# Performance work log

Hardware: AMD Instinct MI355X
Metric: run time of the kernel (lower is better)

## Reference

```python
import jax, jax.numpy as jnp
import numpy as np

EMBED_DIM = 2048
HEAD_DIM = 128
B, T = 4, 2048


def setup_inputs() -> dict:
    key = jax.random.key(0)
    k1, k2, k3, k4 = jax.random.split(key, 4)
    x_in = jax.random.normal(k1, (B, T, EMBED_DIM), dtype=jnp.float32)
    scale = 1.0 / np.sqrt(EMBED_DIM)
    Wq = jax.random.normal(k2, (EMBED_DIM, HEAD_DIM), dtype=jnp.float32) * scale
    Wk = jax.random.normal(k3, (EMBED_DIM, HEAD_DIM), dtype=jnp.float32) * scale
    Wv = jax.random.normal(k4, (EMBED_DIM, HEAD_DIM), dtype=jnp.float32) * scale
    return {"x_in": x_in, "Wq": Wq, "Wk": Wk, "Wv": Wv}


def reference(x_in, Wq, Wk, Wv):
    # x_in: [B, T, E]; projections (Linear, no bias)
    q = jnp.einsum('bte,ed->btd', x_in, Wq)  # [B,T,D]
    k = jnp.einsum('bte,ed->btd', x_in, Wk)
    v = jnp.einsum('bte,ed->btd', x_in, Wv)
    t = x_in.shape[1]
    d = Wq.shape[1]
    s = jnp.einsum('btd,bsd->bts', q, k) / jnp.sqrt(jnp.asarray(d, q.dtype))  # [B,Tq,Tk]
    # causal mask: positions with tril==0 (k index > q index) -> -inf
    causal = jnp.tril(jnp.ones((t, t), dtype=bool))
    s = jnp.where(causal, s, -jnp.inf)
    # NOTE: original module applies softmax over dim=1 (query axis), faithfully reproduced
    a = jax.nn.softmax(s, axis=1)
    z = jnp.einsum('bts,bsd->btd', a, v)  # [B,T,D]
    return z
```

## Files before the change

### kernel.cpp

```cpp
#include <hip/hip_runtime.h>

typedef _Float16 f16x8 __attribute__((ext_vector_type(8)));
typedef _Float16 f16x4 __attribute__((ext_vector_type(4)));
typedef float f32x4 __attribute__((ext_vector_type(4)));

#define T_DIM 2048
#define E_DIM 2048
#define D_DIM 128
#define NB 4
#define KSP_P 4
#define KCH_P 512
#define KSP_A 8
#define KCH_A 256
#define NCH2 32

__device__ __forceinline__ void gll16(const void* g, void* l) {
  __builtin_amdgcn_global_load_lds(
      (const __attribute__((address_space(1))) unsigned int*)g,
      (__attribute__((address_space(3))) unsigned int*)l, 16, 0, 0);
}

__device__ __forceinline__ void merge_stat(float& m, float& l, float pm, float pl) {
  if (pm != -__builtin_inff()) {
    float nm = fmaxf(m, pm);
    l = l * __expf(m - nm) + pl * __expf(pm - nm);
    m = nm;
  }
}


__global__ void cvt_w(const float* __restrict__ Wq, const float* __restrict__ Wk,
                      const float* __restrict__ Wv, _Float16* __restrict__ WhT) {
  int idx = blockIdx.x * 256 + threadIdx.x;
  int w = blockIdx.y;
  const float* W = (w == 0) ? Wq : ((w == 1) ? Wk : Wv);
  int e = idx & (E_DIM - 1), d = idx >> 11;
  WhT[(size_t)w * (D_DIM * E_DIM) + idx] = (_Float16)W[e * D_DIM + d];
}


__global__ __launch_bounds__(768) void proj_gemm(
    const float* __restrict__ x, const _Float16* __restrict__ WhT,
    _Float16* __restrict__ Ph) {
  __shared__ _Float16 A16[2][128 * 32];
  __shared__ _Float16 Bsw[2][384 * 32];
  const int tid = threadIdx.x, w = tid >> 6, lane = tid & 63;
  const int wn = w >> 1, wr = w & 1, quad = lane >> 4, l16 = lane & 15;
  const int t0 = blockIdx.x * 128;
  const int ks = blockIdx.y;
  const int kb = ks * KCH_P;
  const int arowA = tid >> 2, asegA = tid & 3;
  const int br = tid >> 2, bseg = tid & 3;

  f32x4 ax0, ax1;
  auto loadA = [&](int k0) {
    if (tid < 512) {
      const float* src = x + (size_t)(t0 + arowA) * E_DIM + k0 + asegA * 8;
      ax0 = *(const f32x4*)src;
      ax1 = *(const f32x4*)(src + 4);
    }
  };
  auto writeA = [&](int buf) {
    if (tid < 512) {
      f16x8 o;
#pragma unroll
      for (int e = 0; e < 4; ++e) {
        o[e] = (_Float16)ax0[e];
        o[e + 4] = (_Float16)ax1[e];
      }
      *(f16x8*)(&A16[buf][arowA * 32 + asegA * 8]) = o;
    }
  };
  auto stageB = [&](int buf, int k0) {
    int g = bseg ^ ((br >> 1) & 3);
    gll16(WhT + (size_t)br * E_DIM + k0 + g * 8, &Bsw[buf][br * 32 + bseg * 8]);
    int r = 192 + br;
    int g2 = bseg ^ ((r >> 1) & 3);
    gll16(WhT + (size_t)r * E_DIM + k0 + g2 * 8, &Bsw[buf][r * 32 + bseg * 8]);
  };

  f32x4 acc[4][4] = {};
  loadA(kb);
  stageB(0, kb);
  asm volatile("s_waitcnt vmcnt(0)" ::: "memory");
  writeA(0);
  const int NIT = KCH_P / 32;
  for (int it = 0; it < NIT; ++it) {
    const int cur = it & 1;
    __syncthreads();
    if (it + 1 < NIT) {
      loadA(kb + (it + 1) * 32);
      stageB(cur ^ 1, kb + (it + 1) * 32);
    }
    f16x8 af[4], bf[4];
#pragma unroll
    for (int i = 0; i < 4; ++i) {
      int row = wr * 64 + i * 16 + l16;
      af[i] = *(const f16x8*)(&A16[cur][row * 32 + quad * 8]);
    }
#pragma unroll
    for (int j = 0; j < 4; ++j) {
      int row = wn * 64 + j * 16 + l16;
      int sg = quad ^ ((row >> 1) & 3);
      bf[j] = *(const f16x8*)(&Bsw[cur][row * 32 + sg * 8]);
    }
    __builtin_amdgcn_s_setprio(1);
#pragma unroll
    for (int i = 0; i < 4; ++i)
#pragma unroll
      for (int j = 0; j < 4; ++j)
        acc[i][j] = __builtin_amdgcn_mfma_f32_16x16x32_f16(af[i], bf[j], acc[i][j], 0, 0, 0);
    __builtin_amdgcn_s_setprio(0);
    if (it + 1 < NIT) {
      asm volatile("s_waitcnt vmcnt(0)" ::: "memory");
      writeA(cur ^ 1);
    }
  }
  const int mat = wn >> 1;
  const int nb0 = (wn & 1) * 64;
  _Float16* P = Ph + ((size_t)(ks * 3 + mat) << 20);
  if (mat < 2) {
#pragma unroll
    for (int i = 0; i < 4; ++i)
#pragma unroll
      for (int j = 0; j < 4; ++j) {
        int n = nb0 + j * 16 + l16;
#pragma unroll
        for (int r = 0; r < 4; ++r) {
          int t = t0 + wr * 64 + i * 16 + quad * 4 + r;
          P[(size_t)t * D_DIM + n] = (_Float16)acc[i][j][r];
        }
      }
  } else {
#pragma unroll
    for (int i = 0; i < 4; ++i)
#pragma unroll
      for (int j = 0; j < 4; ++j) {
        int n = nb0 + j * 16 + l16;
        int t = t0 + wr * 64 + i * 16 + quad * 4;
        f16x4 o;
#pragma unroll
        for (int r = 0; r < 4; ++r) o[r] = (_Float16)acc[i][j][r];
        *(f16x4*)(P + ((size_t)(t >> 11) * D_DIM + n) * T_DIM + (t & (T_DIM - 1))) = o;
      }
  }
}


__global__ void proj_reduce(const _Float16* __restrict__ Ph, _Float16* __restrict__ Qh,
                            _Float16* __restrict__ Kh, _Float16* __restrict__ VT) {
  size_t u = ((size_t)blockIdx.x * 256 + threadIdx.x) * 8;
  int mat = (int)(u >> 20);
  size_t rem = u & ((1u << 20) - 1);
  float s[8] = {};
#pragma unroll
  for (int ks = 0; ks < KSP_P; ++ks) {
    f16x8 p = *(const f16x8*)(Ph + ((size_t)(ks * 3 + mat) << 20) + rem);
#pragma unroll
    for (int e = 0; e < 8; ++e) s[e] += (float)p[e];
  }
  f16x8 o;
#pragma unroll
  for (int e = 0; e < 8; ++e) o[e] = (_Float16)s[e];
  _Float16* dst = (mat == 0) ? Qh : ((mat == 1) ? Kh : VT);
  *(f16x8*)(dst + rem) = o;
}


__global__ __launch_bounds__(256) void s_gemm(const _Float16* __restrict__ Qh,
                                              const _Float16* __restrict__ Kh,
                                              _Float16* __restrict__ S,
                                              float* __restrict__ Pm,
                                              float* __restrict__ Pl) {
  int idx = blockIdx.x;
  int xt = (int)((sqrtf(8.f * idx + 1.f) - 1.f) * 0.5f);
  while ((xt + 1) * (xt + 2) / 2 <= idx) ++xt;
  while (xt * (xt + 1) / 2 > idx) --xt;
  int yt = idx - xt * (xt + 1) / 2;
  __shared__ _Float16 Bs[4][128 * 32];
  const int tid = threadIdx.x, w = tid >> 6, lane = tid & 63;
  const int wr = w >> 1, wc = w & 1, quad = lane >> 4, l16 = lane & 15;
  const int t0 = xt * 128, s0 = yt * 128, b = blockIdx.y;
  const _Float16* A = Qh + (size_t)b * T_DIM * D_DIM;
  const _Float16* B = Kh + (size_t)b * T_DIM * D_DIM;
  const int srow = lane >> 2;
  const int swz = ((lane & 3) ^ ((srow >> 1) & 3)) * 8;
#pragma unroll
  for (int kq = 0; kq < 4; ++kq)
#pragma unroll
    for (int q = 0; q < 2; ++q) {
      int rbase = w * 32 + q * 16;
      gll16(B + (size_t)(s0 + rbase + srow) * D_DIM + kq * 32 + swz,
            Bs[kq] + rbase * 32);
    }
  __syncthreads();
  f32x4 acc[4][4] = {};
  const int bsg = (quad ^ ((l16 >> 1) & 3)) * 8;
#pragma unroll
  for (int kq = 0; kq < 4; ++kq) {
    f16x8 af[4], bf[4];
#pragma unroll
    for (int i = 0; i < 4; ++i)
      af[i] = *(const f16x8*)(A + (size_t)(t0 + wr * 64 + i * 16 + l16) * D_DIM +
                              kq * 32 + quad * 8);
#pragma unroll
    for (int j = 0; j < 4; ++j)
      bf[j] = *(const f16x8*)(Bs[kq] + (wc * 64 + j * 16 + l16) * 32 + bsg);
#pragma unroll
    for (int i = 0; i < 4; ++i)
#pragma unroll
      for (int j = 0; j < 4; ++j)
        acc[i][j] = __builtin_amdgcn_mfma_f32_16x16x32_f16(af[i], bf[j], acc[i][j], 0, 0, 0);
  }
  _Float16* Sb = S + (size_t)b * T_DIM * T_DIM;
  const float scale = 0.08838834764831845f;
  const float NEG = -__builtin_inff();
#pragma unroll
  for (int j = 0; j < 4; ++j) {
    const int s = s0 + wc * 64 + j * 16 + l16;
    float vv[16];
    float m = NEG;
#pragma unroll
    for (int i = 0; i < 4; ++i)
#pragma unroll
      for (int r = 0; r < 4; ++r) {
        int t = t0 + wr * 64 + i * 16 + quad * 4 + r;
        float v = (s > t) ? NEG : acc[i][j][r] * scale;
        Sb[(size_t)t * T_DIM + s] = (_Float16)v;
        vv[i * 4 + r] = v;
        m = fmaxf(m, v);
      }
    float l = 0.f;
    if (m != NEG) {
#pragma unroll
      for (int k = 0; k < 16; ++k) l += __expf(vv[k] - m);
    }
#pragma unroll
    for (int d = 16; d <= 32; d <<= 1) {
      float pm = __shfl_xor(m, d, 64);
      float pl = __shfl_xor(l, d, 64);
      merge_stat(m, l, pm, pl);
    }
    if (quad == 0) {
      int c = 2 * xt + wr;
      Pm[((size_t)c * NB + b) * T_DIM + s] = m;
      Pl[((size_t)c * NB + b) * T_DIM + s] = l;
    }
  }
}


__global__ __launch_bounds__(256) void comb_stats(const float* __restrict__ Pm,
                                                  const float* __restrict__ Pl,
                                                  float* __restrict__ M,
                                                  float* __restrict__ L) {
  __shared__ float sM[8][32];
  __shared__ float sL[8][32];
  const int g = threadIdx.x >> 5, sl = threadIdx.x & 31;
  const int c = blockIdx.x * 32 + sl;
  const int b = c >> 11, s = c & (T_DIM - 1);
  float m = -__builtin_inff(), l = 0.f;
#pragma unroll
  for (int k = 0; k < NCH2 / 8; ++k) {
    int ch = g * (NCH2 / 8) + k;
    if (ch >= (s >> 6)) {
      size_t idx = ((size_t)ch * NB + b) * T_DIM + s;
      merge_stat(m, l, Pm[idx], Pl[idx]);
    }
  }
  sM[g][sl] = m;
  sL[g][sl] = l;
  __syncthreads();
  if (threadIdx.x < 32) {
    const int c2 = blockIdx.x * 32 + threadIdx.x;
    float fm = -__builtin_inff(), fl = 0.f;
#pragma unroll
    for (int gg = 0; gg < 8; ++gg) merge_stat(fm, fl, sM[gg][threadIdx.x], sL[gg][threadIdx.x]);
    M[c2] = fm;
    L[c2] = 1.f / fl;
  }
}


__global__ __launch_bounds__(256) void av_gemm(const _Float16* __restrict__ S,
                                               const _Float16* __restrict__ VT,
                                               const float* __restrict__ M,
                                               const float* __restrict__ L,
                                               float* __restrict__ Zp) {
  const int t0 = blockIdx.x * 128, b = blockIdx.y, ks = blockIdx.z;
  const int Kmax = t0 + 128;
  const int Kstart = ks * KCH_A;
  if (Kstart >= Kmax) return;
  const int Kend = (Kstart + KCH_A < Kmax) ? (Kstart + KCH_A) : Kmax;
  const int nit = (Kend - Kstart) >> 5;
  __shared__ _Float16 As[2][128 * 32];
  __shared__ _Float16 Bs[2][128 * 32];
  __shared__ float Ms[KCH_A];
  __shared__ float Ls[KCH_A];
  const int tid = threadIdx.x, w = tid >> 6, lane = tid & 63;
  const int wr = w >> 1, wc = w & 1, quad = lane >> 4, l16 = lane & 15;
  const _Float16* Sb = S + (size_t)b * T_DIM * T_DIM;
  const _Float16* Vb = VT + (size_t)b * D_DIM * T_DIM;
  for (int i = tid; i < Kend - Kstart; i += 256) {
    Ms[i] = M[b * T_DIM + Kstart + i];
    Ls[i] = L[b * T_DIM + Kstart + i];
  }
  const int srow = lane >> 2, scol = (lane & 3) * 8;
  const int arow = tid >> 2, ac8 = (tid & 3) * 8;
  f16x8 sv0, sv1;
  auto loadS = [&](int k0) {
    sv0 = *(const f16x8*)(Sb + (size_t)(t0 + arow) * T_DIM + k0 + ac8);
    sv1 = *(const f16x8*)(Sb + (size_t)(t0 + 64 + arow) * T_DIM + k0 + ac8);
  };
  auto stageB = [&](int buf, int k0) {
#pragma unroll
    for (int q = 0; q < 2; ++q) {
      int rbase = w * 32 + q * 16;
      gll16(Vb + (size_t)(rbase + srow) * T_DIM + k0 + scol, Bs[buf] + rbase * 32);
    }
  };
  auto writeA = [&](int buf, int k0) {
#pragma unroll
    for (int q = 0; q < 2; ++q) {
      f16x8 v = q ? sv1 : sv0;
      f16x8 o;
#pragma unroll
      for (int e = 0; e < 8; ++e) {
        int li = k0 + ac8 + e - Kstart;
        o[e] = (_Float16)(__expf((float)v[e] - Ms[li]) * Ls[li]);
      }
      *(f16x8*)(As[buf] + (q * 64 + arow) * 32 + ac8) = o;
    }
  };
  f32x4 acc[4][4] = {};
  __syncthreads();
  loadS(Kstart);
  stageB(0, Kstart);
  asm volatile("s_waitcnt vmcnt(0)" ::: "memory");
  writeA(0, Kstart);
  for (int it = 0; it < nit; ++it) {
    const int cur = it & 1;
    const int k0 = Kstart + it * 32;
    __syncthreads();
    if (it + 1 < nit) {
      loadS(k0 + 32);
      stageB(cur ^ 1, k0 + 32);
    }
    f16x8 af[4], bf[4];
#pragma unroll
    for (int i = 0; i < 4; ++i)
      af[i] = *(const f16x8*)(As[cur] + (wr * 64 + i * 16 + l16) * 32 + quad * 8);
#pragma unroll
    for (int j = 0; j < 4; ++j)
      bf[j] = *(const f16x8*)(Bs[cur] + (wc * 64 + j * 16 + l16) * 32 + quad * 8);
    __builtin_amdgcn_s_setprio(1);
#pragma unroll
    for (int i = 0; i < 4; ++i)
#pragma unroll
      for (int j = 0; j < 4; ++j)
        acc[i][j] = __builtin_amdgcn_mfma_f32_16x16x32_f16(af[i], bf[j], acc[i][j], 0, 0, 0);
    __builtin_amdgcn_s_setprio(0);
    if (it + 1 < nit) {
      asm volatile("s_waitcnt vmcnt(0)" ::: "memory");
      writeA(cur ^ 1, k0 + 32);
    }
  }
  float* Zb = Zp + ((size_t)ks * NB + b) * T_DIM * D_DIM;
#pragma unroll
  for (int i = 0; i < 4; ++i)
#pragma unroll
    for (int j = 0; j < 4; ++j) {
      int n = wc * 64 + j * 16 + l16;
#pragma unroll
      for (int r = 0; r < 4; ++r) {
        int t = t0 + wr * 64 + i * 16 + quad * 4 + r;
        Zb[(size_t)t * D_DIM + n] = acc[i][j][r];
      }
    }
}


__global__ void z_reduce(const float* __restrict__ Zp, float* __restrict__ Z) {
  size_t flat = ((size_t)blockIdx.x * 256 + threadIdx.x) * 4;
  int t = (int)((flat >> 7) & (T_DIM - 1));
  int ns = ((t >> 7) + 2) >> 1;
  f32x4 s = {};
  for (int ks = 0; ks < ns; ++ks) {
    f32x4 p = *(const f32x4*)(Zp + ((size_t)ks * NB * T_DIM * D_DIM) + flat);
    s += p;
  }
  *(f32x4*)(Z + flat) = s;
}


extern "C" void kernel_launch(void* const* d_in, const int* in_sizes, int n_in,
                              void* d_out, int out_size, void* d_ws, size_t ws_size,
                              hipStream_t stream) {
  const float* x = (const float*)d_in[0];
  const float* Wq = (const float*)d_in[1];
  const float* Wk = (const float*)d_in[2];
  const float* Wv = (const float*)d_in[3];
  char* ws = (char*)d_ws;
  float* Zp = (float*)(ws);
  _Float16* WhT = (_Float16*)(ws + 33554432);
  _Float16* Qh = (_Float16*)(ws + 35127296);
  _Float16* Kh = (_Float16*)(ws + 37224448);
  _Float16* VT = (_Float16*)(ws + 39321600);
  _Float16* S = (_Float16*)(ws + 41418752);
  _Float16* Ph = (_Float16*)(ws + 41418752);
  float* M = (float*)(ws + 74973184);
  float* L = (float*)(ws + 75005952);
  float* Pm = (float*)(ws + 75038720);
  float* Pl = (float*)(ws + 76087296);
  float* Z = (float*)d_out;

  cvt_w<<<dim3(1024, 3), 256, 0, stream>>>(Wq, Wk, Wv, WhT);
  proj_gemm<<<dim3(64, KSP_P), 768, 0, stream>>>(x, WhT, Ph);
  proj_reduce<<<1536, 256, 0, stream>>>(Ph, Qh, Kh, VT);
  s_gemm<<<dim3(136, 4), 256, 0, stream>>>(Qh, Kh, S, Pm, Pl);
  comb_stats<<<256, 256, 0, stream>>>(Pm, Pl, M, L);
  av_gemm<<<dim3(16, 4, KSP_A), 256, 0, stream>>>(S, VT, M, L, Zp);
  z_reduce<<<1024, 256, 0, stream>>>(Zp, Z);
}
```

Before: 166.5 us.

## Fuse stats combine into av_gemm, atomically accumulate output, retile projection GEMM

```diff
diff --git a/kernel.cpp b/kernel.cpp
--- a/kernel.cpp
+++ b/kernel.cpp
@@ -29,54 +29,62 @@
 }
 
 
-__global__ void cvt_w(const float* __restrict__ Wq, const float* __restrict__ Wk,
-                      const float* __restrict__ Wv, _Float16* __restrict__ WhT) {
+__global__ void prep(const float* __restrict__ Wq, const float* __restrict__ Wk,
+                     const float* __restrict__ Wv, _Float16* __restrict__ WhT,
+                     float* __restrict__ Z) {
   int idx = blockIdx.x * 256 + threadIdx.x;
-  int w = blockIdx.y;
-  const float* W = (w == 0) ? Wq : ((w == 1) ? Wk : Wv);
-  int e = idx & (E_DIM - 1), d = idx >> 11;
-  WhT[(size_t)w * (D_DIM * E_DIM) + idx] = (_Float16)W[e * D_DIM + d];
-}
-
-
-__global__ __launch_bounds__(768) void proj_gemm(
+  int y = blockIdx.y;
+  if (y < 3) {
+    const float* W = (y == 0) ? Wq : ((y == 1) ? Wk : Wv);
+    int e = idx & (E_DIM - 1), d = idx >> 11;
+    WhT[(size_t)y * (D_DIM * E_DIM) + idx] = (_Float16)W[e * D_DIM + d];
+  } else {
+    f32x4 z = {0.f, 0.f, 0.f, 0.f};
+    *(f32x4*)(Z + (size_t)idx * 4) = z;
+  }
+}
+
+
+__global__ __launch_bounds__(384) void proj_gemm(
     const float* __restrict__ x, const _Float16* __restrict__ WhT,
     _Float16* __restrict__ Ph) {
-  __shared__ _Float16 A16[2][128 * 32];
+  __shared__ _Float16 A16[2][64 * 32];
   __shared__ _Float16 Bsw[2][384 * 32];
   const int tid = threadIdx.x, w = tid >> 6, lane = tid & 63;
-  const int wn = w >> 1, wr = w & 1, quad = lane >> 4, l16 = lane & 15;
-  const int t0 = blockIdx.x * 128;
+  const int wn = w, quad = lane >> 4, l16 = lane & 15;
+  const int t0 = blockIdx.x * 64;
   const int ks = blockIdx.y;
   const int kb = ks * KCH_P;
-  const int arowA = tid >> 2, asegA = tid & 3;
+  const int arow = tid >> 2, aseg = tid & 3;
+  const int asw = (aseg ^ ((arow >> 1) & 3)) * 8;
   const int br = tid >> 2, bseg = tid & 3;
 
   f32x4 ax0, ax1;
   auto loadA = [&](int k0) {
-    if (tid < 512) {
-      const float* src = x + (size_t)(t0 + arowA) * E_DIM + k0 + asegA * 8;
+    if (tid < 256) {
+      const float* src = x + (size_t)(t0 + arow) * E_DIM + k0 + aseg * 8;
       ax0 = *(const f32x4*)src;
       ax1 = *(const f32x4*)(src + 4);
     }
   };
   auto writeA = [&](int buf) {
-    if (tid < 512) {
+    if (tid < 256) {
       f16x8 o;
 #pragma unroll
       for (int e = 0; e < 4; ++e) {
         o[e] = (_Float16)ax0[e];
         o[e + 4] = (_Float16)ax1[e];
       }
-      *(f16x8*)(&A16[buf][arowA * 32 + asegA * 8]) = o;
+      *(f16x8*)(&A16[buf][arow * 32 + asw]) = o;
     }
   };
   auto stageB = [&](int buf, int k0) {
-    int g = bseg ^ ((br >> 1) & 3);
-    gll16(WhT + (size_t)br * E_DIM + k0 + g * 8, &Bsw[buf][br * 32 + bseg * 8]);
-    int r = 192 + br;
-    int g2 = bseg ^ ((r >> 1) & 3);
-    gll16(WhT + (size_t)r * E_DIM + k0 + g2 * 8, &Bsw[buf][r * 32 + bseg * 8]);
+#pragma unroll
+    for (int p = 0; p < 4; ++p) {
+      int r = p * 96 + br;
+      int g = bseg ^ ((r >> 1) & 3);
+      gll16(WhT + (size_t)r * E_DIM + k0 + g * 8, &Bsw[buf][r * 32 + bseg * 8]);
+    }
   };
 
   f32x4 acc[4][4] = {};
@@ -95,14 +103,15 @@
     f16x8 af[4], bf[4];
 #pragma unroll
     for (int i = 0; i < 4; ++i) {
-      int row = wr * 64 + i * 16 + l16;
-      af[i] = *(const f16x8*)(&A16[cur][row * 32 + quad * 8]);
+      int row = i * 16 + l16;
+      int sg = (quad ^ ((row >> 1) & 3)) * 8;
+      af[i] = *(const f16x8*)(&A16[cur][row * 32 + sg]);
     }
 #pragma unroll
     for (int j = 0; j < 4; ++j) {
       int row = wn * 64 + j * 16 + l16;
-      int sg = quad ^ ((row >> 1) & 3);
-      bf[j] = *(const f16x8*)(&Bsw[cur][row * 32 + sg * 8]);
+      int sg = (quad ^ ((row >> 1) & 3)) * 8;
+      bf[j] = *(const f16x8*)(&Bsw[cur][row * 32 + sg]);
     }
     __builtin_amdgcn_s_setprio(1);
 #pragma unroll
@@ -127,7 +136,7 @@
         int n = nb0 + j * 16 + l16;
 #pragma unroll
         for (int r = 0; r < 4; ++r) {
-          int t = t0 + wr * 64 + i * 16 + quad * 4 + r;
+          int t = t0 + i * 16 + quad * 4 + r;
           P[(size_t)t * D_DIM + n] = (_Float16)acc[i][j][r];
         }
       }
@@ -137,7 +146,7 @@
 #pragma unroll
       for (int j = 0; j < 4; ++j) {
         int n = nb0 + j * 16 + l16;
-        int t = t0 + wr * 64 + i * 16 + quad * 4;
+        int t = t0 + i * 16 + quad * 4;
         f16x4 o;
 #pragma unroll
         for (int r = 0; r < 4; ++r) o[r] = (_Float16)acc[i][j][r];
@@ -250,43 +259,11 @@
 }
 
 
-__global__ __launch_bounds__(256) void comb_stats(const float* __restrict__ Pm,
-                                                  const float* __restrict__ Pl,
-                                                  float* __restrict__ M,
-                                                  float* __restrict__ L) {
-  __shared__ float sM[8][32];
-  __shared__ float sL[8][32];
-  const int g = threadIdx.x >> 5, sl = threadIdx.x & 31;
-  const int c = blockIdx.x * 32 + sl;
-  const int b = c >> 11, s = c & (T_DIM - 1);
-  float m = -__builtin_inff(), l = 0.f;
-#pragma unroll
-  for (int k = 0; k < NCH2 / 8; ++k) {
-    int ch = g * (NCH2 / 8) + k;
-    if (ch >= (s >> 6)) {
-      size_t idx = ((size_t)ch * NB + b) * T_DIM + s;
-      merge_stat(m, l, Pm[idx], Pl[idx]);
-    }
-  }
-  sM[g][sl] = m;
-  sL[g][sl] = l;
-  __syncthreads();
-  if (threadIdx.x < 32) {
-    const int c2 = blockIdx.x * 32 + threadIdx.x;
-    float fm = -__builtin_inff(), fl = 0.f;
-#pragma unroll
-    for (int gg = 0; gg < 8; ++gg) merge_stat(fm, fl, sM[gg][threadIdx.x], sL[gg][threadIdx.x]);
-    M[c2] = fm;
-    L[c2] = 1.f / fl;
-  }
-}
-
-
 __global__ __launch_bounds__(256) void av_gemm(const _Float16* __restrict__ S,
                                                const _Float16* __restrict__ VT,
-                                               const float* __restrict__ M,
-                                               const float* __restrict__ L,
-                                               float* __restrict__ Zp) {
+                                               const float* __restrict__ Pm,
+                                               const float* __restrict__ Pl,
+                                               float* __restrict__ Z) {
   const int t0 = blockIdx.x * 128, b = blockIdx.y, ks = blockIdx.z;
   const int Kmax = t0 + 128;
   const int Kstart = ks * KCH_A;
@@ -301,22 +278,41 @@
   const int wr = w >> 1, wc = w & 1, quad = lane >> 4, l16 = lane & 15;
   const _Float16* Sb = S + (size_t)b * T_DIM * T_DIM;
   const _Float16* Vb = VT + (size_t)b * D_DIM * T_DIM;
-  for (int i = tid; i < Kend - Kstart; i += 256) {
-    Ms[i] = M[b * T_DIM + Kstart + i];
-    Ls[i] = L[b * T_DIM + Kstart + i];
-  }
-  const int srow = lane >> 2, scol = (lane & 3) * 8;
-  const int arow = tid >> 2, ac8 = (tid & 3) * 8;
+  {
+    const int s = Kstart + tid;
+    const int c0 = s >> 6;
+    float m = -__builtin_inff(), l = 0.f;
+    for (int base = c0 & ~7; base < NCH2; base += 8) {
+      float pm[8], pl[8];
+#pragma unroll
+      for (int k = 0; k < 8; ++k) {
+        size_t pidx = ((size_t)(base + k) * NB + b) * T_DIM + s;
+        pm[k] = Pm[pidx];
+        pl[k] = Pl[pidx];
+      }
+#pragma unroll
+      for (int k = 0; k < 8; ++k)
+        if (base + k >= c0) merge_stat(m, l, pm[k], pl[k]);
+    }
+    Ms[tid] = m;
+    Ls[tid] = 1.f / l;
+  }
+  __syncthreads();
+  const int srow = lane >> 2;
+  const int arow = tid >> 2, aseg = tid & 3;
+  const int asw = (aseg ^ ((arow >> 1) & 3)) * 8;
   f16x8 sv0, sv1;
   auto loadS = [&](int k0) {
-    sv0 = *(const f16x8*)(Sb + (size_t)(t0 + arow) * T_DIM + k0 + ac8);
-    sv1 = *(const f16x8*)(Sb + (size_t)(t0 + 64 + arow) * T_DIM + k0 + ac8);
+    sv0 = *(const f16x8*)(Sb + (size_t)(t0 + arow) * T_DIM + k0 + aseg * 8);
+    sv1 = *(const f16x8*)(Sb + (size_t)(t0 + 64 + arow) * T_DIM + k0 + aseg * 8);
   };
   auto stageB = [&](int buf, int k0) {
 #pragma unroll
     for (int q = 0; q < 2; ++q) {
       int rbase = w * 32 + q * 16;
-      gll16(Vb + (size_t)(rbase + srow) * T_DIM + k0 + scol, Bs[buf] + rbase * 32);
+      int row = rbase + srow;
+      int g = ((lane & 3) ^ ((row >> 1) & 3)) * 8;
+      gll16(Vb + (size_t)row * T_DIM + k0 + g, Bs[buf] + rbase * 32);
     }
   };
   auto writeA = [&](int buf, int k0) {
@@ -326,14 +322,13 @@
       f16x8 o;
 #pragma unroll
       for (int e = 0; e < 8; ++e) {
-        int li = k0 + ac8 + e - Kstart;
+        int li = k0 + aseg * 8 + e - Kstart;
         o[e] = (_Float16)(__expf((float)v[e] - Ms[li]) * Ls[li]);
       }
-      *(f16x8*)(As[buf] + (q * 64 + arow) * 32 + ac8) = o;
+      *(f16x8*)(As[buf] + (q * 64 + arow) * 32 + asw) = o;
     }
   };
   f32x4 acc[4][4] = {};
-  __syncthreads();
   loadS(Kstart);
   stageB(0, Kstart);
   asm volatile("s_waitcnt vmcnt(0)" ::: "memory");
@@ -348,11 +343,17 @@
     }
     f16x8 af[4], bf[4];
 #pragma unroll
-    for (int i = 0; i < 4; ++i)
-      af[i] = *(const f16x8*)(As[cur] + (wr * 64 + i * 16 + l16) * 32 + quad * 8);
-#pragma unroll
-    for (int j = 0; j < 4; ++j)
-      bf[j] = *(const f16x8*)(Bs[cur] + (wc * 64 + j * 16 + l16) * 32 + quad * 8);
+    for (int i = 0; i < 4; ++i) {
+      int row = wr * 64 + i * 16 + l16;
+      int sg = (quad ^ ((row >> 1) & 3)) * 8;
+      af[i] = *(const f16x8*)(As[cur] + row * 32 + sg);
+    }
+#pragma unroll
+    for (int j = 0; j < 4; ++j) {
+      int row = wc * 64 + j * 16 + l16;
+      int sg = (quad ^ ((row >> 1) & 3)) * 8;
+      bf[j] = *(const f16x8*)(Bs[cur] + row * 32 + sg);
+    }
     __builtin_amdgcn_s_setprio(1);
 #pragma unroll
     for (int i = 0; i < 4; ++i)
@@ -365,7 +366,7 @@
       writeA(cur ^ 1, k0 + 32);
     }
   }
-  float* Zb = Zp + ((size_t)ks * NB + b) * T_DIM * D_DIM;
+  float* Zb = Z + (size_t)b * T_DIM * D_DIM;
 #pragma unroll
   for (int i = 0; i < 4; ++i)
 #pragma unroll
@@ -374,22 +375,9 @@
 #pragma unroll
       for (int r = 0; r < 4; ++r) {
         int t = t0 + wr * 64 + i * 16 + quad * 4 + r;
-        Zb[(size_t)t * D_DIM + n] = acc[i][j][r];
-      }
-    }
-}
-
-
-__global__ void z_reduce(const float* __restrict__ Zp, float* __restrict__ Z) {
-  size_t flat = ((size_t)blockIdx.x * 256 + threadIdx.x) * 4;
-  int t = (int)((flat >> 7) & (T_DIM - 1));
-  int ns = ((t >> 7) + 2) >> 1;
-  f32x4 s = {};
-  for (int ks = 0; ks < ns; ++ks) {
-    f32x4 p = *(const f32x4*)(Zp + ((size_t)ks * NB * T_DIM * D_DIM) + flat);
-    s += p;
-  }
-  *(f32x4*)(Z + flat) = s;
+        atomicAdd(&Zb[(size_t)t * D_DIM + n], acc[i][j][r]);
+      }
+    }
 }
 
 
@@ -401,24 +389,19 @@
   const float* Wk = (const float*)d_in[2];
   const float* Wv = (const float*)d_in[3];
   char* ws = (char*)d_ws;
-  float* Zp = (float*)(ws);
   _Float16* WhT = (_Float16*)(ws + 33554432);
   _Float16* Qh = (_Float16*)(ws + 35127296);
   _Float16* Kh = (_Float16*)(ws + 37224448);
   _Float16* VT = (_Float16*)(ws + 39321600);
   _Float16* S = (_Float16*)(ws + 41418752);
   _Float16* Ph = (_Float16*)(ws + 41418752);
-  float* M = (float*)(ws + 74973184);
-  float* L = (float*)(ws + 75005952);
   float* Pm = (float*)(ws + 75038720);
   float* Pl = (float*)(ws + 76087296);
   float* Z = (float*)d_out;
 
-  cvt_w<<<dim3(1024, 3), 256, 0, stream>>>(Wq, Wk, Wv, WhT);
-  proj_gemm<<<dim3(64, KSP_P), 768, 0, stream>>>(x, WhT, Ph);
+  prep<<<dim3(1024, 4), 256, 0, stream>>>(Wq, Wk, Wv, WhT, Z);
+  proj_gemm<<<dim3(128, KSP_P), 384, 0, stream>>>(x, WhT, Ph);
   proj_reduce<<<1536, 256, 0, stream>>>(Ph, Qh, Kh, VT);
   s_gemm<<<dim3(136, 4), 256, 0, stream>>>(Qh, Kh, S, Pm, Pl);
-  comb_stats<<<256, 256, 0, stream>>>(Pm, Pl, M, L);
-  av_gemm<<<dim3(16, 4, KSP_A), 256, 0, stream>>>(S, VT, M, L, Zp);
-  z_reduce<<<1024, 256, 0, stream>>>(Zp, Z);
-}
+  av_gemm<<<dim3(16, 4, KSP_A), 256, 0, stream>>>(S, VT, Pm, Pl, Z);
+}
```

Result: slower. 185.2 us (+11.2%).
